# Optimization experiments

Measured on AMD Instinct MI355X. Metric: run time of the kernel, lower is better.

## Reference

```python
import jax, jax.numpy as jnp
import numpy as np

B, N, C, H = 8, 2048, 512, 8
D = C // H                      # head dim = 64
Q_LENGTHS = [1024 + 128 * i for i in range(B)]  # ragged: 1024..1920, sum below
TQ = sum(Q_LENGTHS)             # 11776 total queries


def setup_inputs() -> dict:
    key = jax.random.key(0)
    ks = jax.random.split(key, 5)
    w = 0.02  # init scale for weights
    return {
        "x": jax.random.normal(ks[0], (B, N, C), jnp.float32),
        "q": jax.random.normal(ks[1], (TQ, C), jnp.float32),
        "Wq": jax.random.normal(ks[2], (C, C), jnp.float32) * w,
        "Wkv": jax.random.normal(ks[3], (2 * C, C), jnp.float32) * w,
        "Wproj": jax.random.normal(ks[4], (C, C), jnp.float32) * w,
        "bproj": jnp.zeros((C,), jnp.float32),
        "q_lengths": jnp.array(Q_LENGTHS, jnp.int32),
        "max_q_len": max(Q_LENGTHS),
    }


def reference(x, q, Wq, Wkv, Wproj, bproj, q_lengths, max_q_len):
    # Eval path of Attention.forward: batched_sparse_attention(q, k, v, q_lengths, scale)
    # == varlen cross-attention: queries of batch b attend over all N kv tokens of batch b.
    Tq = q.shape[0]
    scale = D ** -0.5

    qh = (q @ Wq.T).reshape(Tq, H, D)                 # [Tq, H, D]
    kv = (x @ Wkv.T).reshape(B, N, 2, H, D)
    k = kv[:, :, 0]                                   # [B, N, H, D]
    v = kv[:, :, 1]                                   # [B, N, H, D]

    # ragged -> padded per-batch layout
    csum = jnp.cumsum(q_lengths)                      # [B]
    offs = jnp.concatenate([jnp.zeros((1,), csum.dtype), csum])
    tok = jnp.arange(Tq)
    q_batch = (tok[:, None] >= csum[None, :]).sum(-1)  # [Tq] batch id per query
    q_pos = tok - offs[q_batch]                        # [Tq] position within batch

    qpad = jnp.zeros((B, max_q_len, H, D), qh.dtype).at[q_batch, q_pos].set(qh)

    scores = jnp.einsum('blhd,bnhd->bhln', qpad, k) * scale  # [B, H, L, N]
    attn = jax.nn.softmax(scores, axis=-1)                   # all N keys valid
    out = jnp.einsum('bhln,bnhd->blhd', attn, v)             # [B, L, H, D]

    out = out[q_batch, q_pos].reshape(Tq, C)           # gather ragged rows back
    return out @ Wproj.T + bproj
```

## Files before the change

### kernel.cpp

```cpp
#include <hip/hip_runtime.h>
#include <hip/hip_bf16.h>
#include <math.h>

constexpr int Cc = 512;
constexpr int Hh = 8;
constexpr int Dd = 64;
constexpr int Nn = 2048;
constexpr int Bb = 8;
constexpr int GK = 512;

typedef __attribute__((ext_vector_type(8))) short short8;
typedef __attribute__((ext_vector_type(4))) float f32x4;
typedef __attribute__((ext_vector_type(4))) unsigned int u32x4;
typedef __attribute__((ext_vector_type(2))) unsigned int u32x2;

#define C2SCALE 0.1803368801f

static __device__ __forceinline__ ushort f2bf(float v) {
  __hip_bfloat16 h = __float2bfloat16(v);
  return *reinterpret_cast<ushort*>(&h);
}
static __device__ __forceinline__ float bf2f(ushort u) {
  __hip_bfloat16 h = *reinterpret_cast<__hip_bfloat16*>(&u);
  return __bfloat162float(h);
}
static __device__ __forceinline__ unsigned int pk2(float f0, float f1) {
  return (unsigned int)f2bf(f0) | ((unsigned int)f2bf(f1) << 16);
}

template <int MODE, int TERMS, bool AF32, bool BF32>
__global__ __launch_bounds__(256) void mfma_nt2_kernel(
    const void* __restrict__ A0p, const void* __restrict__ A1p,
    const void* __restrict__ B0p, const void* __restrict__ B1p,
    const float* __restrict__ bias, float* __restrict__ Cf,
    ushort* __restrict__ Chi, int Nc)
{
  __shared__ ushort lAh[128 * 32];
  __shared__ ushort lBh[128 * 32];
  __shared__ ushort lAl[TERMS == 3 ? 128 * 32 : 1];
  __shared__ ushort lBl[TERMS == 3 ? 128 * 32 : 1];

  const int tid = threadIdx.x;
  const int w = tid >> 6, lane = tid & 63;
  const int c = lane & 15, g = lane >> 4;
  const int wr = (w >> 1) * 64, wc = (w & 1) * 64;
  const int m0 = blockIdx.y * 128, n0 = blockIdx.x * 128;
  const int sr = tid >> 2;
  const int sk = (tid & 3) * 8;

  short8 rAh[2], rAl[2], rBh[2], rBl[2];

  auto ldf32 = [&](const float* F, size_t idx, short8& h, short8& l) {
    const float4 f0 = *(const float4*)(F + idx);
    const float4 f1 = *(const float4*)(F + idx + 4);
    const float vv[8] = {f0.x, f0.y, f0.z, f0.w, f1.x, f1.y, f1.z, f1.w};
#pragma unroll
    for (int j = 0; j < 8; ++j) {
      const ushort hb = f2bf(vv[j]);
      ((ushort*)&h)[j] = hb;
      if (TERMS == 3) ((ushort*)&l)[j] = f2bf(vv[j] - bf2f(hb));
    }
  };

  auto loadA = [&](int k0) {
#pragma unroll
    for (int hf = 0; hf < 2; ++hf) {
      const size_t idx = (size_t)(m0 + sr + hf * 64) * GK + k0 + sk;
      if (AF32) {
        ldf32((const float*)A0p, idx, rAh[hf], rAl[hf]);
      } else {
        rAh[hf] = *(const short8*)((const ushort*)A0p + idx);
        if (TERMS == 3) rAl[hf] = *(const short8*)((const ushort*)A1p + idx);
      }
    }
  };
  auto loadB = [&](int k0) {
#pragma unroll
    for (int hf = 0; hf < 2; ++hf) {
      const size_t idx = (size_t)(n0 + sr + hf * 64) * GK + k0 + sk;
      if (BF32) {
        ldf32((const float*)B0p, idx, rBh[hf], rBl[hf]);
      } else {
        rBh[hf] = *(const short8*)((const ushort*)B0p + idx);
        if (TERMS == 3) rBl[hf] = *(const short8*)((const ushort*)B1p + idx);
      }
    }
  };

  f32x4 acc[4][4] = {};
  loadA(0);
  loadB(0);

  for (int k0 = 0; k0 < GK; k0 += 32) {
    __syncthreads();
    *(short8*)&lAh[sr * 32 + sk]        = rAh[0];
    *(short8*)&lAh[(sr + 64) * 32 + sk] = rAh[1];
    *(short8*)&lBh[sr * 32 + sk]        = rBh[0];
    *(short8*)&lBh[(sr + 64) * 32 + sk] = rBh[1];
    if (TERMS == 3) {
      *(short8*)&lAl[sr * 32 + sk]        = rAl[0];
      *(short8*)&lAl[(sr + 64) * 32 + sk] = rAl[1];
      *(short8*)&lBl[sr * 32 + sk]        = rBl[0];
      *(short8*)&lBl[(sr + 64) * 32 + sk] = rBl[1];
    }
    __syncthreads();
    if (k0 + 32 < GK) { loadA(k0 + 32); loadB(k0 + 32); }

    short8 ah[4], al[4], bh[4], bl[4];
#pragma unroll
    for (int i = 0; i < 4; ++i) {
      const int ar = (wr + i * 16 + c) * 32 + g * 8;
      const int br = (wc + i * 16 + c) * 32 + g * 8;
      ah[i] = *(const short8*)&lAh[ar];
      bh[i] = *(const short8*)&lBh[br];
      if (TERMS == 3) {
        al[i] = *(const short8*)&lAl[ar];
        bl[i] = *(const short8*)&lBl[br];
      }
    }
#pragma unroll
    for (int mi = 0; mi < 4; ++mi)
#pragma unroll
      for (int nj = 0; nj < 4; ++nj) {
        if (TERMS == 3) {
          acc[mi][nj] = __builtin_amdgcn_mfma_f32_16x16x32_bf16(ah[mi], bl[nj], acc[mi][nj], 0,0,0);
          acc[mi][nj] = __builtin_amdgcn_mfma_f32_16x16x32_bf16(al[mi], bh[nj], acc[mi][nj], 0,0,0);
        }
        acc[mi][nj] = __builtin_amdgcn_mfma_f32_16x16x32_bf16(ah[mi], bh[nj], acc[mi][nj], 0,0,0);
      }
  }

#pragma unroll
  for (int mi = 0; mi < 4; ++mi) {
#pragma unroll
    for (int r = 0; r < 4; ++r) {
      const size_t rb = (size_t)(m0 + wr + mi * 16 + g * 4 + r) * Nc;
#pragma unroll
      for (int nj = 0; nj < 4; ++nj) {
        const int col = n0 + wc + nj * 16 + c;
        const float v = acc[mi][nj][r];
        if (MODE == 0) {
          Cf[rb + col] = v + bias[col];
        } else if (MODE == 1) {
          Chi[rb + col] = f2bf(v);
        } else {
          Chi[rb + col] = f2bf(v * C2SCALE);
        }
      }
    }
  }
}

__global__ __launch_bounds__(256, 4) void attn_mfma12_kernel(
    const ushort* __restrict__ qhi,
    const ushort* __restrict__ kbf,
    const ushort* __restrict__ vtb,
    ushort* __restrict__ ohi,
    ushort* __restrict__ olo)
{
  constexpr int QOFF[8] = {0, 1024, 2176, 3456, 4864, 6400, 8064, 9856};

  const int lin = blockIdx.x;
  const int b  = lin & 7;
  const int h  = (lin >> 3) & 7;
  const int qt = lin >> 6;

  const int Lb  = 1024 + 128 * b;
  const int off = QOFF[b];
  if (qt * 128 >= Lb) return;

  constexpr int KP = 72;
  constexpr int VP = 136;
  constexpr int NC = Nn / 128;
  __shared__ ushort Ks[128 * KP];
  __shared__ ushort Vs[64 * VP];

  const int tid = threadIdx.x;
  const int lane = tid & 63;
  const int w = tid >> 6;
  const int c = lane & 15;
  const int g = (lane >> 4) & 3;

  short8 qf[2][2];
  int qrow[2];
#pragma unroll
  for (int t = 0; t < 2; ++t) {
    qrow[t] = off + qt * 128 + w * 32 + t * 16 + c;
    const size_t base = (size_t)qrow[t] * Cc + h * Dd + g * 8;
    qf[t][0] = *(const short8*)(qhi + base);
    qf[t][1] = *(const short8*)(qhi + base + 32);
  }

  float l_part[2] = {0.f, 0.f};
  f32x4 accO4[2][4] = {};

  const size_t kbase = (size_t)b * Nn * Cc + h * Dd;
  const size_t vbase = (size_t)h * Dd * (Bb * Nn) + (size_t)b * Nn;

  for (int ch = 0; ch < NC; ++ch) {
    __syncthreads();
#pragma unroll
    for (int it = 0; it < 4; ++it) {
      const int i = tid + it * 256;
      const int row = i >> 3, c8 = (i & 7) * 8;
      *(short8*)&Ks[row * KP + c8] =
          *(const short8*)&kbf[kbase + (size_t)(ch * 128 + row) * Cc + c8];
    }
#pragma unroll
    for (int it = 0; it < 4; ++it) {
      const int i = tid + it * 256;
      const int row = i >> 4, c8 = (i & 15) * 8;
      const int kb1 = (c8 & ~31) | (((c8 >> 3) & 3) << 2);
      const size_t gb = vbase + (size_t)row * (Bb * Nn) + ch * 128;
      const u32x2 vlo = *(const u32x2*)&vtb[gb + kb1];
      const u32x2 vhi = *(const u32x2*)&vtb[gb + kb1 + 16];
      u32x4 vv;
      vv[0] = vlo[0]; vv[1] = vlo[1];
      vv[2] = vhi[0]; vv[3] = vhi[1];
      *(short8*)&Vs[row * VP + c8] = __builtin_bit_cast(short8, vv);
    }
    __syncthreads();

#pragma unroll
    for (int st = 0; st < 2; ++st) {
      f32x4 accT4[2][4] = {};
      __builtin_amdgcn_s_setprio(1);
#pragma unroll
      for (int ks2 = 0; ks2 < 2; ++ks2) {
#pragma unroll
        for (int kb = 0; kb < 4; ++kb) {
          const short8 kf = *(const short8*)
              &Ks[(st * 64 + kb * 16 + c) * KP + ks2 * 32 + g * 8];
          accT4[0][kb] = __builtin_amdgcn_mfma_f32_16x16x32_bf16(kf, qf[0][ks2], accT4[0][kb], 0,0,0);
          accT4[1][kb] = __builtin_amdgcn_mfma_f32_16x16x32_bf16(kf, qf[1][ks2], accT4[1][kb], 0,0,0);
        }
      }
      __builtin_amdgcn_s_setprio(0);

      unsigned int up[2][4][2];
#pragma unroll
      for (int t = 0; t < 2; ++t)
#pragma unroll
        for (int kb = 0; kb < 4; ++kb) {
          const float p0 = __builtin_amdgcn_exp2f(accT4[t][kb][0]);
          const float p1 = __builtin_amdgcn_exp2f(accT4[t][kb][1]);
          const float p2 = __builtin_amdgcn_exp2f(accT4[t][kb][2]);
          const float p3 = __builtin_amdgcn_exp2f(accT4[t][kb][3]);
          l_part[t] += (p0 + p1) + (p2 + p3);
          up[t][kb][0] = pk2(p0, p1);
          up[t][kb][1] = pk2(p2, p3);
        }

#pragma unroll
      for (int ks2 = 0; ks2 < 2; ++ks2) {
        short8 pa[2];
#pragma unroll
        for (int t = 0; t < 2; ++t) {
          u32x4 wv;
          wv.x = up[t][2 * ks2][0];
          wv.y = up[t][2 * ks2][1];
          wv.z = up[t][2 * ks2 + 1][0];
          wv.w = up[t][2 * ks2 + 1][1];
          pa[t] = __builtin_bit_cast(short8, wv);
        }
        __builtin_amdgcn_s_setprio(1);
#pragma unroll
        for (int db = 0; db < 4; ++db) {
          const short8 vf = *(const short8*)
              &Vs[(db * 16 + c) * VP + st * 64 + ks2 * 32 + g * 8];
          accO4[0][db] = __builtin_amdgcn_mfma_f32_16x16x32_bf16(vf, pa[0], accO4[0][db], 0,0,0);
          accO4[1][db] = __builtin_amdgcn_mfma_f32_16x16x32_bf16(vf, pa[1], accO4[1][db], 0,0,0);
        }
        __builtin_amdgcn_s_setprio(0);
      }
    }
  }

#pragma unroll
  for (int t = 0; t < 2; ++t) {
    float l = l_part[t];
    l += __shfl_xor(l, 16);
    l += __shfl_xor(l, 32);
    const float inv = 1.f / l;
    const size_t rb = (size_t)qrow[t] * Cc + h * Dd;
#pragma unroll
    for (int db = 0; db < 4; ++db) {
      const int d0 = db * 16 + g * 4;
      ushort4 uh, ul;
#pragma unroll
      for (int e = 0; e < 4; ++e) {
        const float o = accO4[t][db][e] * inv;
        const ushort hb = f2bf(o);
        ((ushort*)&uh)[e] = hb;
        ((ushort*)&ul)[e] = f2bf(o - bf2f(hb));
      }
      *(ushort4*)&ohi[rb + d0] = uh;
      *(ushort4*)&olo[rb + d0] = ul;
    }
  }
}

extern "C" void kernel_launch(void* const* d_in, const int* in_sizes, int n_in,
                              void* d_out, int out_size, void* d_ws, size_t ws_size,
                              hipStream_t stream)
{
  const float* x     = (const float*)d_in[0];
  const float* q     = (const float*)d_in[1];
  const float* Wq    = (const float*)d_in[2];
  const float* Wkv   = (const float*)d_in[3];
  const float* Wproj = (const float*)d_in[4];
  const float* bproj = (const float*)d_in[5];

  const int TQ = in_sizes[1] / Cc;
  const int BN = in_sizes[0] / Cc;

  const float* Wv = Wkv + (size_t)Cc * Cc;

  const size_t szQ = (size_t)TQ * Cc * 2;
  const size_t szX = (size_t)BN * Cc * 2;

  char* p = (char*)d_ws;
  ushort* q_hi  = (ushort*)p;  p += szQ;
  ushort* k_bf  = (ushort*)p;  p += szX;
  ushort* v_t   = (ushort*)p;  p += szX;
  ushort* at_hi = (ushort*)p;  p += szQ;
  ushort* at_lo = (ushort*)p;

  mfma_nt2_kernel<2, 1, true, true><<<dim3(Cc/128, TQ/128), 256, 0, stream>>>(
      q, nullptr, Wq, nullptr, nullptr, nullptr, q_hi, Cc);
  mfma_nt2_kernel<1, 1, true, true><<<dim3(Cc/128, BN/128), 256, 0, stream>>>(
      x, nullptr, Wkv, nullptr, nullptr, nullptr, k_bf, Cc);
  mfma_nt2_kernel<1, 1, true, true><<<dim3(BN/128, Cc/128), 256, 0, stream>>>(
      Wv, nullptr, x, nullptr, nullptr, nullptr, v_t, BN);
  attn_mfma12_kernel<<<dim3(64 * 15), 256, 0, stream>>>(
      q_hi, k_bf, v_t, at_hi, at_lo);
  mfma_nt2_kernel<0, 3, false, true><<<dim3(Cc/128, TQ/128), 256, 0, stream>>>(
      at_hi, at_lo, Wproj, nullptr, bproj, (float*)d_out, nullptr, Cc);
}
```

Baseline: 186.4 us.

## Fuse K and V projections into one GEMM and prefetch attention KV tiles

Replaces the two separate K and V projection GEMM launches with one fused kernel. It reads each x tile once, computes K and V accumulators together, and writes V transposed through an LDS staging buffer. The attention kernel now loads the next K/V chunk into registers while the current chunk is being computed, overlapping global loads with MFMA work. The cost is higher register pressure: two 4x4 accumulator sets in the fused GEMM at lower occupancy, plus extra prefetch registers in attention.

```diff
diff --git a/kernel.cpp b/kernel.cpp
--- a/kernel.cpp
+++ b/kernel.cpp
@@ -151,7 +151,110 @@
   }
 }
 
-__global__ __launch_bounds__(256, 4) void attn_mfma12_kernel(
+__global__ __launch_bounds__(256, 2) void mfma_kv_fused_kernel(
+    const float* __restrict__ x, const float* __restrict__ Wkv,
+    ushort* __restrict__ kbf, ushort* __restrict__ vtb, int BN)
+{
+  __shared__ ushort smem[128 * 136];
+  ushort* lA   = smem;
+  ushort* lBk  = smem + 128 * 32;
+  ushort* lBv  = smem + 2 * 128 * 32;
+  ushort* tbuf = smem;
+
+  const int tid = threadIdx.x;
+  const int w = tid >> 6, lane = tid & 63;
+  const int c = lane & 15, g = lane >> 4;
+  const int wr = (w >> 1) * 64, wc = (w & 1) * 64;
+  const int n0 = blockIdx.x * 128, m0 = blockIdx.y * 128;
+  const int sr = tid >> 2, sk = (tid & 3) * 8;
+
+  auto cvt8 = [&](const float* F, size_t idx) -> short8 {
+    const float4 f0 = *(const float4*)(F + idx);
+    const float4 f1 = *(const float4*)(F + idx + 4);
+    const float vv[8] = {f0.x, f0.y, f0.z, f0.w, f1.x, f1.y, f1.z, f1.w};
+    short8 h;
+#pragma unroll
+    for (int j = 0; j < 8; ++j) ((ushort*)&h)[j] = f2bf(vv[j]);
+    return h;
+  };
+
+  short8 rA[2], rBk[2], rBv[2];
+  auto loadAll = [&](int k0) {
+#pragma unroll
+    for (int hf = 0; hf < 2; ++hf) {
+      rA[hf]  = cvt8(x,   (size_t)(m0 + sr + hf * 64) * GK + k0 + sk);
+      rBk[hf] = cvt8(Wkv, (size_t)(n0 + sr + hf * 64) * GK + k0 + sk);
+      rBv[hf] = cvt8(Wkv, (size_t)(512 + n0 + sr + hf * 64) * GK + k0 + sk);
+    }
+  };
+
+  f32x4 ak[4][4] = {};
+  f32x4 av[4][4] = {};
+  loadAll(0);
+
+  for (int k0 = 0; k0 < GK; k0 += 32) {
+    __syncthreads();
+    *(short8*)&lA[sr * 32 + sk]         = rA[0];
+    *(short8*)&lA[(sr + 64) * 32 + sk]  = rA[1];
+    *(short8*)&lBk[sr * 32 + sk]        = rBk[0];
+    *(short8*)&lBk[(sr + 64) * 32 + sk] = rBk[1];
+    *(short8*)&lBv[sr * 32 + sk]        = rBv[0];
+    *(short8*)&lBv[(sr + 64) * 32 + sk] = rBv[1];
+    __syncthreads();
+    if (k0 + 32 < GK) loadAll(k0 + 32);
+
+    short8 a[4], bk[4], bv[4];
+#pragma unroll
+    for (int i = 0; i < 4; ++i) {
+      const int ar = (wr + i * 16 + c) * 32 + g * 8;
+      const int br = (wc + i * 16 + c) * 32 + g * 8;
+      a[i]  = *(const short8*)&lA[ar];
+      bk[i] = *(const short8*)&lBk[br];
+      bv[i] = *(const short8*)&lBv[br];
+    }
+#pragma unroll
+    for (int mi = 0; mi < 4; ++mi)
+#pragma unroll
+      for (int nj = 0; nj < 4; ++nj) {
+        ak[mi][nj] = __builtin_amdgcn_mfma_f32_16x16x32_bf16(a[mi], bk[nj], ak[mi][nj], 0,0,0);
+        av[mi][nj] = __builtin_amdgcn_mfma_f32_16x16x32_bf16(a[mi], bv[nj], av[mi][nj], 0,0,0);
+      }
+  }
+
+#pragma unroll
+  for (int mi = 0; mi < 4; ++mi)
+#pragma unroll
+    for (int r = 0; r < 4; ++r) {
+      const size_t rb = (size_t)(m0 + wr + mi * 16 + g * 4 + r) * Cc;
+#pragma unroll
+      for (int nj = 0; nj < 4; ++nj)
+        kbf[rb + n0 + wc + nj * 16 + c] = f2bf(ak[mi][nj][r]);
+    }
+
+  __syncthreads();
+#pragma unroll
+  for (int mi = 0; mi < 4; ++mi)
+#pragma unroll
+    for (int r = 0; r < 4; ++r) {
+      const int tl = wr + mi * 16 + g * 4 + r;
+#pragma unroll
+      for (int nj = 0; nj < 4; ++nj) {
+        const int dl = wc + nj * 16 + c;
+        tbuf[dl * 136 + tl] = f2bf(av[mi][nj][r]);
+      }
+    }
+  __syncthreads();
+#pragma unroll
+  for (int it = 0; it < 8; ++it) {
+    const int idx = tid + it * 256;
+    const int row = idx >> 4;
+    const int c8 = (idx & 15) * 8;
+    *(short8*)&vtb[(size_t)(n0 + row) * BN + m0 + c8] =
+        *(const short8*)&tbuf[row * 136 + c8];
+  }
+}
+
+__global__ __launch_bounds__(256, 4) void attn_mfma13_kernel(
     const ushort* __restrict__ qhi,
     const ushort* __restrict__ kbf,
     const ushort* __restrict__ vtb,
@@ -197,15 +300,16 @@
   const size_t kbase = (size_t)b * Nn * Cc + h * Dd;
   const size_t vbase = (size_t)h * Dd * (Bb * Nn) + (size_t)b * Nn;
 
-  for (int ch = 0; ch < NC; ++ch) {
-    __syncthreads();
+  short8 rk[4], rv[4];
+  auto loadK = [&](int ch) {
 #pragma unroll
     for (int it = 0; it < 4; ++it) {
       const int i = tid + it * 256;
       const int row = i >> 3, c8 = (i & 7) * 8;
-      *(short8*)&Ks[row * KP + c8] =
-          *(const short8*)&kbf[kbase + (size_t)(ch * 128 + row) * Cc + c8];
-    }
+      rk[it] = *(const short8*)&kbf[kbase + (size_t)(ch * 128 + row) * Cc + c8];
+    }
+  };
+  auto loadV = [&](int ch) {
 #pragma unroll
     for (int it = 0; it < 4; ++it) {
       const int i = tid + it * 256;
@@ -217,9 +321,27 @@
       u32x4 vv;
       vv[0] = vlo[0]; vv[1] = vlo[1];
       vv[2] = vhi[0]; vv[3] = vhi[1];
-      *(short8*)&Vs[row * VP + c8] = __builtin_bit_cast(short8, vv);
-    }
-    __syncthreads();
+      rv[it] = __builtin_bit_cast(short8, vv);
+    }
+  };
+
+  loadK(0);
+  loadV(0);
+
+  for (int ch = 0; ch < NC; ++ch) {
+    __syncthreads();
+#pragma unroll
+    for (int it = 0; it < 4; ++it) {
+      const int i = tid + it * 256;
+      *(short8*)&Ks[(i >> 3) * KP + (i & 7) * 8] = rk[it];
+    }
+#pragma unroll
+    for (int it = 0; it < 4; ++it) {
+      const int i = tid + it * 256;
+      *(short8*)&Vs[(i >> 4) * VP + (i & 15) * 8] = rv[it];
+    }
+    __syncthreads();
+    if (ch + 1 < NC) { loadK(ch + 1); loadV(ch + 1); }
 
 #pragma unroll
     for (int st = 0; st < 2; ++st) {
@@ -314,8 +436,6 @@
   const int TQ = in_sizes[1] / Cc;
   const int BN = in_sizes[0] / Cc;
 
-  const float* Wv = Wkv + (size_t)Cc * Cc;
-
   const size_t szQ = (size_t)TQ * Cc * 2;
   const size_t szX = (size_t)BN * Cc * 2;
 
@@ -328,11 +448,9 @@
 
   mfma_nt2_kernel<2, 1, true, true><<<dim3(Cc/128, TQ/128), 256, 0, stream>>>(
       q, nullptr, Wq, nullptr, nullptr, nullptr, q_hi, Cc);
-  mfma_nt2_kernel<1, 1, true, true><<<dim3(Cc/128, BN/128), 256, 0, stream>>>(
-      x, nullptr, Wkv, nullptr, nullptr, nullptr, k_bf, Cc);
-  mfma_nt2_kernel<1, 1, true, true><<<dim3(BN/128, Cc/128), 256, 0, stream>>>(
-      Wv, nullptr, x, nullptr, nullptr, nullptr, v_t, BN);
-  attn_mfma12_kernel<<<dim3(64 * 15), 256, 0, stream>>>(
+  mfma_kv_fused_kernel<<<dim3(Cc/128, BN/128), 256, 0, stream>>>(
+      x, Wkv, k_bf, v_t, BN);
+  attn_mfma13_kernel<<<dim3(64 * 15), 256, 0, stream>>>(
       q_hi, k_bf, v_t, at_hi, at_lo);
   mfma_nt2_kernel<0, 3, false, true><<<dim3(Cc/128, TQ/128), 256, 0, stream>>>(
       at_hi, at_lo, Wproj, nullptr, bproj, (float*)d_out, nullptr, Cc);
```

Measured after the change: 302.9 us. +62.5%, slower.
